# Performance work log

Measured on AMD Instinct MI355X. Metric: run time of the kernel, lower is better.

The kernel has to match this reference:

```python
import jax, jax.numpy as jnp
import numpy as np

N_NODES = 100000
N_EDGES = 300000
N_TYPES = 3
HID = 128
EMB = 64
N_GRAPHS = 4096
T_STEPS = 4


def setup_inputs() -> dict:
    key = jax.random.key(0)
    ks = jax.random.split(key, 12)
    s = 1.0 / np.sqrt(HID)
    return {
        "node_features": jax.random.normal(ks[0], (N_NODES, HID), jnp.float32),
        "edge_index": jax.random.randint(ks[1], (N_TYPES, 2, N_EDGES), 0, N_NODES),
        "node_to_graph_id": jnp.sort(jax.random.randint(ks[2], (N_NODES,), 0, N_GRAPHS)),
        "W_msg": jax.random.normal(ks[3], (N_TYPES, HID, HID), jnp.float32) * s,
        "b_msg": jnp.zeros((N_TYPES, HID), jnp.float32),
        "W_ih": jax.random.normal(ks[4], (3 * HID, HID), jnp.float32) * s,
        "W_hh": jax.random.normal(ks[5], (3 * HID, HID), jnp.float32) * s,
        "b_ih": jnp.zeros((3 * HID,), jnp.float32),
        "b_hh": jnp.zeros((3 * HID,), jnp.float32),
        "W_proj": jax.random.normal(ks[6], (EMB, HID), jnp.float32) * s,
        "b_proj": jnp.zeros((EMB,), jnp.float32),
        "W_gate": jax.random.normal(ks[7], (EMB, HID), jnp.float32) * s,
        "b_gate": jnp.zeros((EMB,), jnp.float32),
    }


def _gru_cell(m, h, W_ih, W_hh, b_ih, b_hh):
    # torch.nn.GRUCell math; gates ordered (r, z, n)
    gi = m @ W_ih.T + b_ih          # [N, 3H]
    gh = h @ W_hh.T + b_hh          # [N, 3H]
    i_r, i_z, i_n = jnp.split(gi, 3, axis=-1)
    h_r, h_z, h_n = jnp.split(gh, 3, axis=-1)
    r = jax.nn.sigmoid(i_r + h_r)
    z = jax.nn.sigmoid(i_z + h_z)
    n = jnp.tanh(i_n + r * h_n)
    return (1.0 - z) * n + z * h


def reference(node_features, edge_index, node_to_graph_id,
              W_msg, b_msg, W_ih, W_hh, b_ih, b_hh,
              W_proj, b_proj, W_gate, b_gate):
    h = node_features  # [N, H]

    def per_type(eidx, W, b, h):
        src, dst = eidx[0], eidx[1]
        m = h[src] @ W + b  # gather + per-edge-type linear, [E, H]
        return jax.ops.segment_sum(m, dst, num_segments=N_NODES)

    for _ in range(T_STEPS):  # fixed small T: python loop is fine
        msgs = jax.vmap(per_type, in_axes=(0, 0, 0, None))(edge_index, W_msg, b_msg, h)
        m = msgs.sum(axis=0)  # [N, H] aggregated over edge types
        h = _gru_cell(m, h, W_ih, W_hh, b_ih, b_hh)

    # gated index_add graph readout (mlp_down is identity)
    proj = h @ W_proj.T + b_proj                 # [N, E]
    gate = jax.nn.sigmoid(h @ W_gate.T + b_gate)  # [N, E]
    graph_feats = jax.ops.segment_sum(gate * proj, node_to_graph_id,
                                      num_segments=N_GRAPHS)
    return graph_feats
```

## Files before the change

kernel.cpp:

```cpp
#include <hip/hip_runtime.h>
#include <hip/hip_bf16.h>
#include <math.h>

#define NN 100000
#define NNP 100096
#define NE 300000
#define HID 128
#define EMB 64
#define NG 4096
#define DEG_CAP 32
#define XS 512

typedef __bf16 bf16x8 __attribute__((ext_vector_type(8)));
typedef float  f32x16 __attribute__((ext_vector_type(16)));
typedef short  short8 __attribute__((ext_vector_type(8)));

typedef const __attribute__((address_space(1))) unsigned int* gas_u32;
typedef __attribute__((address_space(3))) unsigned int* las_u32;

__device__ __forceinline__ void gload16(const void* g, void* l) {
    __builtin_amdgcn_global_load_lds((gas_u32)g, (las_u32)l, 16, 0, 0);
}

__device__ __forceinline__ float bf2f(unsigned short u) {
    unsigned int x = ((unsigned int)u) << 16;
    return __builtin_bit_cast(float, x);
}
__device__ __forceinline__ unsigned short f2bf(float f) {
    unsigned int x = __builtin_bit_cast(unsigned int, f);
    unsigned int r = x + 0x7fff + ((x >> 16) & 1);
    return (unsigned short)(r >> 16);
}
__device__ __forceinline__ float sigm(float x) { return 1.f / (1.f + __expf(-x)); }

__global__ __launch_bounds__(256) void k_init(const float* __restrict__ nf,
                                              unsigned short* __restrict__ Y,
                                              unsigned short* __restrict__ X) {
    int id = blockIdx.x * 256 + threadIdx.x;
    int n = id >> 7, c = id & 127;
    unsigned short hv = (n < NN) ? f2bf(nf[(long)n * HID + c]) : (unsigned short)0;
    Y[(long)n * HID + c] = hv;
    X[(long)n * XS + 384 + c] = hv;
}

__global__ __launch_bounds__(256) void k_build_csr(const int* __restrict__ ei,
                                                   int* __restrict__ deg,
                                                   int* __restrict__ csr) {
    int id = blockIdx.x * 256 + threadIdx.x;
    if (id >= 3 * NE) return;
    int t = id / NE;
    int i = id - t * NE;
    int src = ei[(t * 2 + 0) * NE + i];
    int dst = ei[(t * 2 + 1) * NE + i];
    int p = atomicAdd(&deg[t * NN + dst], 1);
    if (p < DEG_CAP) csr[((long)t * NN + dst) * DEG_CAP + p] = src;
}

__global__ __launch_bounds__(256) void k_pack_deg(const int* __restrict__ deg,
                                                  int4* __restrict__ degp) {
    int n = blockIdx.x * 256 + threadIdx.x;
    if (n >= NNP) return;
    int4 v; v.x = 0; v.y = 0; v.z = 0; v.w = 0;
    if (n < NN) { v.x = deg[n]; v.y = deg[NN + n]; v.z = deg[2 * NN + n]; }
    degp[n] = v;
}

__global__ __launch_bounds__(512) void k_build_w(const float* __restrict__ Wmsg,
                                                 const float* __restrict__ Wih,
                                                 const float* __restrict__ Whh,
                                                 unsigned short* __restrict__ Bf) {
    int np = blockIdx.x;
    int k = threadIdx.x;
    int c = np >> 2, sec = np & 3;
    float v = 0.f;
    if (k < 384) {
        if (sec < 3) {
            int t = k >> 7, kk = k & 127;
            const float* wm = Wmsg + ((long)t * HID + kk) * HID;
            const float* wi = Wih + (long)(sec * HID + c) * HID;
            float s = 0.f;
            for (int j = 0; j < HID; j++) s += wm[j] * wi[j];
            v = s;
        }
    } else {
        int kk = k - 384;
        if (sec == 0)      v = Whh[(long)c * HID + kk];
        else if (sec == 1) v = Whh[(long)(HID + c) * HID + kk];
        else if (sec == 3) v = Whh[(long)(2 * HID + c) * HID + kk];
    }
    int nb = np >> 5, nl = np & 31;
    int k16 = k >> 4, kgg = (k >> 3) & 1, e = k & 7;
    Bf[((((nb * 32 + k16) * 2 + kgg) * 32 + nl) << 3) + e] = f2bf(v);
}

__global__ __launch_bounds__(512) void k_build_bias(const float* __restrict__ bih,
                                                    const float* __restrict__ bhh,
                                                    const float* __restrict__ bmsg,
                                                    const float* __restrict__ Wih,
                                                    float* __restrict__ bbig,
                                                    float* __restrict__ Bdeg) {
    int np = threadIdx.x;
    int c = np >> 2, sec = np & 3;
    float b;
    if (sec == 0)      b = bih[c] + bhh[c];
    else if (sec == 1) b = bih[HID + c] + bhh[HID + c];
    else if (sec == 2) b = bih[2 * HID + c];
    else               b = bhh[2 * HID + c];
    bbig[np] = b;
    for (int t = 0; t < 3; t++) {
        float s = 0.f;
        if (sec < 3) {
            const float* wi = Wih + (long)(sec * HID + c) * HID;
            const float* bm = bmsg + t * HID;
            for (int j = 0; j < HID; j++) s += bm[j] * wi[j];
        }
        Bdeg[t * 512 + np] = s;
    }
}

__global__ __launch_bounds__(256) void k_agg(const unsigned short* __restrict__ Y,
                                             unsigned short* __restrict__ X,
                                             const int* __restrict__ deg,
                                             const int* __restrict__ csr) {
    const int lane = threadIdx.x & 63;
    const long n = (long)blockIdx.x * 4 + (threadIdx.x >> 6);
    const int g = lane >> 4;
    const int c16 = lane & 15;
    const int l31 = lane & 31;

    int d[3], il[3];
#pragma unroll
    for (int t = 0; t < 3; t++) {
        int dt = deg[t * NN + n];
        d[t] = dt > DEG_CAP ? DEG_CAP : dt;
        il[t] = csr[((long)t * NN + n) * DEG_CAP + l31];
    }
#pragma unroll
    for (int t = 0; t < 3; t++) {
        float acc[8] = {0.f, 0.f, 0.f, 0.f, 0.f, 0.f, 0.f, 0.f};
        int rounds = (d[t] + 3) >> 2;
        for (int r = 0; r < rounds; r++) {
            int j = r * 4 + g;
            int idx = __shfl(il[t], j & 31);
            if (j < d[t]) {
                short8 v = *(const short8*)(Y + (long)idx * HID + c16 * 8);
#pragma unroll
                for (int q = 0; q < 8; q++) acc[q] += bf2f((unsigned short)v[q]);
            }
        }
#pragma unroll
        for (int q = 0; q < 8; q++) {
            acc[q] += __shfl_xor(acc[q], 16);
            acc[q] += __shfl_xor(acc[q], 32);
        }
        if (g == 0) {
            short8 o;
#pragma unroll
            for (int q = 0; q < 8; q++) o[q] = (short)f2bf(acc[q]);
            *(short8*)(X + n * XS + t * HID + c16 * 8) = o;
        }
    }
}

__global__ __launch_bounds__(512, 2) void k_gru_mfma(
        const unsigned short* __restrict__ X,
        unsigned short* __restrict__ Xh,
        const unsigned short* __restrict__ Y,
        unsigned short* __restrict__ Yw,
        const unsigned short* __restrict__ Bf,
        const float* __restrict__ bbig, const float* __restrict__ Bdeg,
        const int4* __restrict__ degp) {
    __shared__ char lds[65536];

    const int tid = threadIdx.x;
    const int lane = tid & 63;
    const int wv = tid >> 6;
    const int wr = wv >> 2;
    const int wc = wv & 3;
    const int r31 = lane & 31;
    const int kg = lane >> 5;
    const long row0 = (long)blockIdx.x * 128;

    f32x16 acc[2][4];
#pragma unroll
    for (int i = 0; i < 2; i++)
#pragma unroll
        for (int j = 0; j < 4; j++) acc[i][j] = (f32x16)(0.0f);

    const char* pA = (const char*)X + (row0 + lane) * 1024;
#define STAGE_A(H)                                                              \
    {                                                                           \
        _Pragma("unroll")                                                       \
        for (int jj = 0; jj < 8; jj++) {                                        \
            gload16(pA + ((jj & 1) * 65536 + (H) * 512 +                        \
                          (wv * 2 + (jj >> 2)) * 32 + ((jj >> 1) & 1) * 16),    \
                    lds + (wv * 8 + jj) * 1024);                                \
        }                                                                       \
    }

    const unsigned short* pB0 = Bf + (wc * 4 + 0) * 16384 + lane * 8;
    const unsigned short* pB1 = Bf + (wc * 4 + 1) * 16384 + lane * 8;
    const unsigned short* pB2 = Bf + (wc * 4 + 2) * 16384 + lane * 8;
    const unsigned short* pB3 = Bf + (wc * 4 + 3) * 16384 + lane * 8;

    const int vAoff = kg * 2048 + wr * 1024 + r31 * 16;
    const char* ldsA = lds;

    STAGE_A(0);
    __syncthreads();

#pragma unroll
    for (int it = 0; it < 16; it++) {
        if (it == 8) {
            __syncthreads();
            STAGE_A(1);
            __syncthreads();
        }
#pragma unroll
        for (int kb = 0; kb < 2; kb++) {
            const int kl = (it & 7) * 2 + kb;
            const int k16 = it * 2 + kb;
            short8 af0 = *(const short8*)(ldsA + kl * 4096 + vAoff);
            short8 af1 = *(const short8*)(ldsA + kl * 4096 + 512 + vAoff);
            short8 b0 = *(const short8*)(pB0 + k16 * 512);
            short8 b1 = *(const short8*)(pB1 + k16 * 512);
            short8 b2 = *(const short8*)(pB2 + k16 * 512);
            short8 b3 = *(const short8*)(pB3 + k16 * 512);
            acc[0][0] = __builtin_amdgcn_mfma_f32_32x32x16_bf16(
                __builtin_bit_cast(bf16x8, af0), __builtin_bit_cast(bf16x8, b0), acc[0][0], 0, 0, 0);
            acc[0][1] = __builtin_amdgcn_mfma_f32_32x32x16_bf16(
                __builtin_bit_cast(bf16x8, af0), __builtin_bit_cast(bf16x8, b1), acc[0][1], 0, 0, 0);
            acc[0][2] = __builtin_amdgcn_mfma_f32_32x32x16_bf16(
                __builtin_bit_cast(bf16x8, af0), __builtin_bit_cast(bf16x8, b2), acc[0][2], 0, 0, 0);
            acc[0][3] = __builtin_amdgcn_mfma_f32_32x32x16_bf16(
                __builtin_bit_cast(bf16x8, af0), __builtin_bit_cast(bf16x8, b3), acc[0][3], 0, 0, 0);
            acc[1][0] = __builtin_amdgcn_mfma_f32_32x32x16_bf16(
                __builtin_bit_cast(bf16x8, af1), __builtin_bit_cast(bf16x8, b0), acc[1][0], 0, 0, 0);
            acc[1][1] = __builtin_amdgcn_mfma_f32_32x32x16_bf16(
                __builtin_bit_cast(bf16x8, af1), __builtin_bit_cast(bf16x8, b1), acc[1][1], 0, 0, 0);
            acc[1][2] = __builtin_amdgcn_mfma_f32_32x32x16_bf16(
                __builtin_bit_cast(bf16x8, af1), __builtin_bit_cast(bf16x8, b2), acc[1][2], 0, 0, 0);
            acc[1][3] = __builtin_amdgcn_mfma_f32_32x32x16_bf16(
                __builtin_bit_cast(bf16x8, af1), __builtin_bit_cast(bf16x8, b3), acc[1][3], 0, 0, 0);
        }
    }

    float* EX = (float*)lds;
    const int ch = tid & 127;
    const int rbase = tid >> 7;
    const float4 bb = *(const float4*)(bbig + ch * 4);
    const float4 e0 = *(const float4*)(Bdeg + ch * 4);
    const float4 e1 = *(const float4*)(Bdeg + 512 + ch * 4);
    const float4 e2 = *(const float4*)(Bdeg + 1024 + ch * 4);

#pragma unroll
    for (int b = 0; b < 4; b++) {
        __syncthreads();
        if (wr == (b >> 1)) {
            const int rt = b & 1;
#pragma unroll
            for (int ct = 0; ct < 4; ct++) {
                int col = wc * 128 + ct * 32 + r31;
#pragma unroll
                for (int q = 0; q < 16; q++) {
                    int rw = (q & 3) + 8 * (q >> 2) + 4 * kg;
                    EX[rw * 512 + col] = acc[rt][ct][q];
                }
            }
        }
        __syncthreads();
#pragma unroll
        for (int i = 0; i < 8; i++) {
            int rw = rbase + 4 * i;
            long grow = row0 + b * 32 + rw;
            int4 dg = degp[grow];
            float dgx = (float)dg.x, dgy = (float)dg.y, dgz = (float)dg.z;
            float4 v = *(const float4*)(EX + rw * 512 + ch * 4);
            float Sr = v.x + bb.x + dgx * e0.x + dgy * e1.x + dgz * e2.x;
            float Sz = v.y + bb.y + dgx * e0.y + dgy * e1.y + dgz * e2.y;
            float In = v.z + bb.z + dgx * e0.z + dgy * e1.z + dgz * e2.z;
            float Hn = v.w + bb.w;
            float rr = sigm(Sr);
            float zz = sigm(Sz);
            float tt = In + rr * Hn;
            float ee = __expf(2.f * tt);
            float nn = 1.f - 2.f / (ee + 1.f);
            float hv = (1.f - zz) * nn + zz * bf2f(Y[grow * HID + ch]);
            unsigned short hb = f2bf(hv);
            Yw[grow * HID + ch] = hb;
            Xh[grow * XS + 384 + ch] = hb;
        }
    }
}

__global__ __launch_bounds__(256) void k_readout(const unsigned short* __restrict__ Y,
                                                 const int* __restrict__ n2g,
                                                 const float* __restrict__ Wp,
                                                 const float* __restrict__ bp,
                                                 const float* __restrict__ Wg,
                                                 const float* __restrict__ bg,
                                                 float* __restrict__ out) {
    __shared__ float hs[32][132];
    __shared__ float Ws[64][129];
    int tid = threadIdx.x;
    long row0 = (long)blockIdx.x * 32;
    int rg = tid >> 5, cg = tid & 31;
    float acc[4][4];
#pragma unroll
    for (int r = 0; r < 4; r++)
#pragma unroll
        for (int c = 0; c < 4; c++) acc[r][c] = 0.f;

#pragma unroll
    for (int p = 0; p < 2; p++) {
        int e = p * 256 + tid;
        int r = e >> 4, c8 = e & 15;
        short8 v = *(const short8*)(Y + (row0 + r) * HID + c8 * 8);
#pragma unroll
        for (int j = 0; j < 8; j++) hs[r][c8 * 8 + j] = bf2f((unsigned short)v[j]);
    }
    for (int kc = 0; kc < 128; kc += 64) {
        __syncthreads();
#pragma unroll
        for (int p = 0; p < 8; p++) {
            int idx = p * 256 + tid;
            int j = idx >> 4, q = idx & 15;
            const float* Wsrc = (j < 64) ? Wp : Wg;
            float4 w = *(const float4*)&Wsrc[(j & 63) * HID + kc + q * 4];
            Ws[q * 4 + 0][j] = w.x;
            Ws[q * 4 + 1][j] = w.y;
            Ws[q * 4 + 2][j] = w.z;
            Ws[q * 4 + 3][j] = w.w;
        }
        __syncthreads();
#pragma unroll 8
        for (int k = 0; k < 64; k++) {
            float a[4], w[4];
#pragma unroll
            for (int r = 0; r < 4; r++) a[r] = hs[rg * 4 + r][kc + k];
#pragma unroll
            for (int c = 0; c < 4; c++) w[c] = Ws[k][cg + 32 * c];
#pragma unroll
            for (int r = 0; r < 4; r++)
#pragma unroll
                for (int c = 0; c < 4; c++) acc[r][c] += a[r] * w[c];
        }
    }
#pragma unroll
    for (int r = 0; r < 4; r++) {
        long row = row0 + rg * 4 + r;
        if (row < NN) {
            int g = n2g[row];
            float pv0 = acc[r][0] + bp[cg];
            float pv1 = acc[r][1] + bp[cg + 32];
            float gv0 = acc[r][2] + bg[cg];
            float gv1 = acc[r][3] + bg[cg + 32];
            atomicAdd(&out[g * EMB + cg],      pv0 * sigm(gv0));
            atomicAdd(&out[g * EMB + cg + 32], pv1 * sigm(gv1));
        }
    }
}

extern "C" void kernel_launch(void* const* d_in, const int* in_sizes, int n_in,
                              void* d_out, int out_size, void* d_ws, size_t ws_size,
                              hipStream_t stream) {
    const float* node_features = (const float*)d_in[0];
    const int*   edge_index    = (const int*)d_in[1];
    const int*   n2g           = (const int*)d_in[2];
    const float* W_msg         = (const float*)d_in[3];
    const float* b_msg         = (const float*)d_in[4];
    const float* W_ih          = (const float*)d_in[5];
    const float* W_hh          = (const float*)d_in[6];
    const float* b_ih          = (const float*)d_in[7];
    const float* b_hh          = (const float*)d_in[8];
    const float* W_proj        = (const float*)d_in[9];
    const float* b_proj        = (const float*)d_in[10];
    const float* W_gate        = (const float*)d_in[11];
    const float* b_gate        = (const float*)d_in[12];

    char* ws = (char*)d_ws;
    unsigned short* X    = (unsigned short*)(ws);
    unsigned short* Y    = (unsigned short*)(ws + 102498304);
    unsigned short* Bf   = (unsigned short*)(ws + 128122880);
    float*          bbig = (float*)         (ws + 128647168);
    float*          Bdeg = (float*)         (ws + 128649216);
    int4*           degp = (int4*)          (ws + 128655360);
    int*            deg  = (int*)           (ws + 130256896);
    int*            csr  = (int*)           (ws + 131456896);

    float* out = (float*)d_out;

    hipMemsetAsync(out, 0, (size_t)NG * EMB * sizeof(float), stream);
    hipMemsetAsync(deg, 0, (size_t)3 * NN * sizeof(int), stream);

    k_init<<<dim3((NNP * HID) / 256), dim3(256), 0, stream>>>(node_features, Y, X);
    k_build_csr<<<dim3((3 * NE + 255) / 256), dim3(256), 0, stream>>>(edge_index, deg, csr);
    k_pack_deg<<<dim3(NNP / 256), dim3(256), 0, stream>>>(deg, degp);
    k_build_w<<<dim3(512), dim3(512), 0, stream>>>(W_msg, W_ih, W_hh, Bf);
    k_build_bias<<<dim3(1), dim3(512), 0, stream>>>(b_ih, b_hh, b_msg, W_ih, bbig, Bdeg);

    for (int step = 0; step < 4; step++) {
        k_agg<<<dim3(NN / 4), dim3(256), 0, stream>>>(Y, X, deg, csr);
        k_gru_mfma<<<dim3(NNP / 128), dim3(512), 0, stream>>>(X, X, Y, Y, Bf,
                                                              bbig, Bdeg, degp);
    }
    k_readout<<<dim3(NN / 32), dim3(256), 0, stream>>>(Y, n2g, W_proj, b_proj,
                                                       W_gate, b_gate, out);
}
```

Measured before the change: 928.3 us.

## Halve GRU MFMA row tile to 64 and raise occupancy to four blocks

```diff
diff --git a/kernel.cpp b/kernel.cpp
--- a/kernel.cpp
+++ b/kernel.cpp
@@ -162,7 +162,7 @@
     }
 }
 
-__global__ __launch_bounds__(512, 2) void k_gru_mfma(
+__global__ __launch_bounds__(512, 4) void k_gru_mfma(
         const unsigned short* __restrict__ X,
         unsigned short* __restrict__ Xh,
         const unsigned short* __restrict__ Y,
@@ -170,79 +170,73 @@
         const unsigned short* __restrict__ Bf,
         const float* __restrict__ bbig, const float* __restrict__ Bdeg,
         const int4* __restrict__ degp) {
-    __shared__ char lds[65536];
+    __shared__ char lds[32768];
 
     const int tid = threadIdx.x;
     const int lane = tid & 63;
     const int wv = tid >> 6;
-    const int wr = wv >> 2;
-    const int wc = wv & 3;
     const int r31 = lane & 31;
     const int kg = lane >> 5;
-    const long row0 = (long)blockIdx.x * 128;
-
-    f32x16 acc[2][4];
+    const long row0 = (long)blockIdx.x * 64;
+
+    f32x16 acc[2][2];
 #pragma unroll
     for (int i = 0; i < 2; i++)
 #pragma unroll
-        for (int j = 0; j < 4; j++) acc[i][j] = (f32x16)(0.0f);
-
-    const char* pA = (const char*)X + (row0 + lane) * 1024;
-#define STAGE_A(H)                                                              \
+        for (int j = 0; j < 2; j++) acc[i][j] = (f32x16)(0.0f);
+
+    const char* pAl = (const char*)X + (row0 + r31) * 1024 + kg * 16;
+#define STAGE_A(HALF)                                                           \
     {                                                                           \
         _Pragma("unroll")                                                       \
-        for (int jj = 0; jj < 8; jj++) {                                        \
-            gload16(pA + ((jj & 1) * 65536 + (H) * 512 +                        \
-                          (wv * 2 + (jj >> 2)) * 32 + ((jj >> 1) & 1) * 16),    \
-                    lds + (wv * 8 + jj) * 1024);                                \
+        for (int jj = 0; jj < 4; jj++) {                                        \
+            const int f = wv * 4 + jj;                                          \
+            gload16(pAl + (f & 1) * 32768 + ((HALF) * 16 + (f >> 1)) * 32,      \
+                    lds + f * 1024);                                            \
         }                                                                       \
     }
 
-    const unsigned short* pB0 = Bf + (wc * 4 + 0) * 16384 + lane * 8;
-    const unsigned short* pB1 = Bf + (wc * 4 + 1) * 16384 + lane * 8;
-    const unsigned short* pB2 = Bf + (wc * 4 + 2) * 16384 + lane * 8;
-    const unsigned short* pB3 = Bf + (wc * 4 + 3) * 16384 + lane * 8;
-
-    const int vAoff = kg * 2048 + wr * 1024 + r31 * 16;
-    const char* ldsA = lds;
+    const unsigned short* pB0 = Bf + (wv * 2 + 0) * 16384 + lane * 8;
+    const unsigned short* pB1 = Bf + (wv * 2 + 1) * 16384 + lane * 8;
 
     STAGE_A(0);
     __syncthreads();
 
 #pragma unroll
-    for (int it = 0; it < 16; it++) {
-        if (it == 8) {
-            __syncthreads();
-            STAGE_A(1);
-            __syncthreads();
-        }
-#pragma unroll
-        for (int kb = 0; kb < 2; kb++) {
-            const int kl = (it & 7) * 2 + kb;
-            const int k16 = it * 2 + kb;
-            short8 af0 = *(const short8*)(ldsA + kl * 4096 + vAoff);
-            short8 af1 = *(const short8*)(ldsA + kl * 4096 + 512 + vAoff);
-            short8 b0 = *(const short8*)(pB0 + k16 * 512);
-            short8 b1 = *(const short8*)(pB1 + k16 * 512);
-            short8 b2 = *(const short8*)(pB2 + k16 * 512);
-            short8 b3 = *(const short8*)(pB3 + k16 * 512);
-            acc[0][0] = __builtin_amdgcn_mfma_f32_32x32x16_bf16(
-                __builtin_bit_cast(bf16x8, af0), __builtin_bit_cast(bf16x8, b0), acc[0][0], 0, 0, 0);
-            acc[0][1] = __builtin_amdgcn_mfma_f32_32x32x16_bf16(
-                __builtin_bit_cast(bf16x8, af0), __builtin_bit_cast(bf16x8, b1), acc[0][1], 0, 0, 0);
-            acc[0][2] = __builtin_amdgcn_mfma_f32_32x32x16_bf16(
-                __builtin_bit_cast(bf16x8, af0), __builtin_bit_cast(bf16x8, b2), acc[0][2], 0, 0, 0);
-            acc[0][3] = __builtin_amdgcn_mfma_f32_32x32x16_bf16(
-                __builtin_bit_cast(bf16x8, af0), __builtin_bit_cast(bf16x8, b3), acc[0][3], 0, 0, 0);
-            acc[1][0] = __builtin_amdgcn_mfma_f32_32x32x16_bf16(
-                __builtin_bit_cast(bf16x8, af1), __builtin_bit_cast(bf16x8, b0), acc[1][0], 0, 0, 0);
-            acc[1][1] = __builtin_amdgcn_mfma_f32_32x32x16_bf16(
-                __builtin_bit_cast(bf16x8, af1), __builtin_bit_cast(bf16x8, b1), acc[1][1], 0, 0, 0);
-            acc[1][2] = __builtin_amdgcn_mfma_f32_32x32x16_bf16(
-                __builtin_bit_cast(bf16x8, af1), __builtin_bit_cast(bf16x8, b2), acc[1][2], 0, 0, 0);
-            acc[1][3] = __builtin_amdgcn_mfma_f32_32x32x16_bf16(
-                __builtin_bit_cast(bf16x8, af1), __builtin_bit_cast(bf16x8, b3), acc[1][3], 0, 0, 0);
-        }
+    for (int k16l = 0; k16l < 16; k16l++) {
+        short8 a0 = *(const short8*)(lds + (k16l * 2 + 0) * 1024 + lane * 16);
+        short8 a1 = *(const short8*)(lds + (k16l * 2 + 1) * 1024 + lane * 16);
+        short8 b0 = *(const short8*)(pB0 + k16l * 512);
+        short8 b1 = *(const short8*)(pB1 + k16l * 512);
+        acc[0][0] = __builtin_amdgcn_mfma_f32_32x32x16_bf16(
+            __builtin_bit_cast(bf16x8, a0), __builtin_bit_cast(bf16x8, b0), acc[0][0], 0, 0, 0);
+        acc[0][1] = __builtin_amdgcn_mfma_f32_32x32x16_bf16(
+            __builtin_bit_cast(bf16x8, a0), __builtin_bit_cast(bf16x8, b1), acc[0][1], 0, 0, 0);
+        acc[1][0] = __builtin_amdgcn_mfma_f32_32x32x16_bf16(
+            __builtin_bit_cast(bf16x8, a1), __builtin_bit_cast(bf16x8, b0), acc[1][0], 0, 0, 0);
+        acc[1][1] = __builtin_amdgcn_mfma_f32_32x32x16_bf16(
+            __builtin_bit_cast(bf16x8, a1), __builtin_bit_cast(bf16x8, b1), acc[1][1], 0, 0, 0);
+    }
+
+    __syncthreads();
+    STAGE_A(1);
+    __syncthreads();
+
+#pragma unroll
+    for (int k16l = 0; k16l < 16; k16l++) {
+        const int k16g = 16 + k16l;
+        short8 a0 = *(const short8*)(lds + (k16l * 2 + 0) * 1024 + lane * 16);
+        short8 a1 = *(const short8*)(lds + (k16l * 2 + 1) * 1024 + lane * 16);
+        short8 b0 = *(const short8*)(pB0 + k16g * 512);
+        short8 b1 = *(const short8*)(pB1 + k16g * 512);
+        acc[0][0] = __builtin_amdgcn_mfma_f32_32x32x16_bf16(
+            __builtin_bit_cast(bf16x8, a0), __builtin_bit_cast(bf16x8, b0), acc[0][0], 0, 0, 0);
+        acc[0][1] = __builtin_amdgcn_mfma_f32_32x32x16_bf16(
+            __builtin_bit_cast(bf16x8, a0), __builtin_bit_cast(bf16x8, b1), acc[0][1], 0, 0, 0);
+        acc[1][0] = __builtin_amdgcn_mfma_f32_32x32x16_bf16(
+            __builtin_bit_cast(bf16x8, a1), __builtin_bit_cast(bf16x8, b0), acc[1][0], 0, 0, 0);
+        acc[1][1] = __builtin_amdgcn_mfma_f32_32x32x16_bf16(
+            __builtin_bit_cast(bf16x8, a1), __builtin_bit_cast(bf16x8, b1), acc[1][1], 0, 0, 0);
     }
 
     float* EX = (float*)lds;
@@ -256,26 +250,27 @@
 #pragma unroll
     for (int b = 0; b < 4; b++) {
         __syncthreads();
-        if (wr == (b >> 1)) {
-            const int rt = b & 1;
-#pragma unroll
-            for (int ct = 0; ct < 4; ct++) {
-                int col = wc * 128 + ct * 32 + r31;
-#pragma unroll
-                for (int q = 0; q < 16; q++) {
-                    int rw = (q & 3) + 8 * (q >> 2) + 4 * kg;
-                    EX[rw * 512 + col] = acc[rt][ct][q];
+        {
+            const int mt = b >> 1;
+            const int qh = (b & 1) * 8;
+#pragma unroll
+            for (int ct = 0; ct < 2; ct++) {
+                int col = wv * 64 + ct * 32 + r31;
+#pragma unroll
+                for (int qq = 0; qq < 8; qq++) {
+                    int rwl = (qq & 3) + 8 * (qq >> 2) + 4 * kg;
+                    EX[rwl * 512 + col] = acc[mt][ct][qh + qq];
                 }
             }
         }
         __syncthreads();
 #pragma unroll
-        for (int i = 0; i < 8; i++) {
-            int rw = rbase + 4 * i;
-            long grow = row0 + b * 32 + rw;
+        for (int i = 0; i < 4; i++) {
+            int rwl = rbase + 4 * i;
+            long grow = row0 + b * 16 + rwl;
             int4 dg = degp[grow];
             float dgx = (float)dg.x, dgy = (float)dg.y, dgz = (float)dg.z;
-            float4 v = *(const float4*)(EX + rw * 512 + ch * 4);
+            float4 v = *(const float4*)(EX + rwl * 512 + ch * 4);
             float Sr = v.x + bb.x + dgx * e0.x + dgy * e1.x + dgz * e2.x;
             float Sz = v.y + bb.y + dgx * e0.y + dgy * e1.y + dgz * e2.y;
             float In = v.z + bb.z + dgx * e0.z + dgy * e1.z + dgz * e2.z;
@@ -401,8 +396,8 @@
 
     for (int step = 0; step < 4; step++) {
         k_agg<<<dim3(NN / 4), dim3(256), 0, stream>>>(Y, X, deg, csr);
-        k_gru_mfma<<<dim3(NNP / 128), dim3(512), 0, stream>>>(X, X, Y, Y, Bf,
-                                                              bbig, Bdeg, degp);
+        k_gru_mfma<<<dim3(NNP / 64), dim3(512), 0, stream>>>(X, X, Y, Y, Bf,
+                                                             bbig, Bdeg, degp);
     }
     k_readout<<<dim3(NN / 32), dim3(256), 0, stream>>>(Y, n2g, W_proj, b_proj,
                                                        W_gate, b_gate, out);
```

After: 824.1 us. -11.2%, faster.
